# Performance work log

Measured on AMD Instinct MI355X. Metric: run time of the kernel, lower is better.

## Reference

```python
import jax, jax.numpy as jnp
import numpy as np

N_NODES = 50000
N_EDGES = 800000
IN_DIM, HID_DIM, N_CLASS = 128, 128, 2
DROPOUT_P = 0.5
NEG_SLOPE = 0.01  # F.leaky_relu default


def gcn_conv(x, src, dst, W, b, n_nodes):
    """PyG GCNConv: add self-loops, sym-normalize, aggregate, then bias."""
    loops = jnp.arange(n_nodes, dtype=src.dtype)
    s = jnp.concatenate([src, loops])
    d = jnp.concatenate([dst, loops])
    # degree on A + I (edge weights = 1), counted at destination
    deg = jax.ops.segment_sum(jnp.ones_like(d, dtype=x.dtype), d, num_segments=n_nodes)
    dis = jnp.where(deg > 0, jax.lax.rsqrt(deg), 0.0)  # deg^{-1/2}
    norm = dis[s] * dis[d]                               # [E+N]
    h = x @ W                                            # [N, out]
    msg = h[s] * norm[:, None]                           # gather + scale
    out = jax.ops.segment_sum(msg, d, num_segments=n_nodes)  # scatter-add
    return out + b


def dropout(x, p, key):
    keep = 1.0 - p
    mask = jax.random.bernoulli(key, keep, x.shape)
    return jnp.where(mask, x / keep, 0.0)


def setup_inputs() -> dict:
    key = jax.random.key(0)
    ks = jax.random.split(key, 8)
    x = jax.random.normal(ks[0], (N_NODES, IN_DIM), dtype=jnp.float32)
    edge_index = jax.random.randint(ks[1], (2, N_EDGES), 0, N_NODES, dtype=jnp.int64)
    def glorot(k, fin, fout):
        lim = np.sqrt(6.0 / (fin + fout)).astype(np.float32)
        return jax.random.uniform(k, (fin, fout), jnp.float32, -lim, lim)
    W1 = glorot(ks[2], IN_DIM, HID_DIM)
    W2 = glorot(ks[3], HID_DIM, HID_DIM)
    W3 = glorot(ks[4], HID_DIM, N_CLASS)
    b1 = jnp.zeros((HID_DIM,), jnp.float32)
    b2 = jnp.zeros((HID_DIM,), jnp.float32)
    b3 = jnp.zeros((N_CLASS,), jnp.float32)
    return {"x": x, "edge_index": edge_index, "W1": W1, "b1": b1,
            "W2": W2, "b2": b2, "W3": W3, "b3": b3}


def reference(x, edge_index, W1, b1, W2, b2, W3, b3):
    src, dst = edge_index[0], edge_index[1]
    n = x.shape[0]
    dkey = jax.random.key(42)
    k1, k2 = jax.random.split(dkey)
    h = gcn_conv(x, src, dst, W1, b1, n)
    h = jax.nn.leaky_relu(h, NEG_SLOPE)
    h = dropout(h, DROPOUT_P, k1)
    h = gcn_conv(h, src, dst, W2, b2, n)
    h = jax.nn.leaky_relu(h, NEG_SLOPE)
    h = dropout(h, DROPOUT_P, k2)
    h = gcn_conv(h, src, dst, W3, b3, n)
    return jax.nn.log_softmax(h, axis=1)
```

## Files before the change

kernel.cpp:

```cpp
#include <hip/hip_runtime.h>
#include <stdint.h>

#define N_NODES 50000
#define N_EDGES 800000
#define DIM     128
#define NB   196
#define CAP  8192
#define CHUNK 2048
#define NBLK 391
#define GNODES 16
#define GGRID 3125
#define GCAP2 2048
#define G3CAP 8192
#define ZBLK 98

typedef __attribute__((ext_vector_type(8))) unsigned short ushort8_t;
typedef __attribute__((ext_vector_type(8))) short bfrag;
typedef __attribute__((ext_vector_type(4))) float f32x4;

__host__ __device__ inline void threefry2x32(uint32_t k0, uint32_t k1,
                                             uint32_t x0, uint32_t x1,
                                             uint32_t& o0, uint32_t& o1) {
    uint32_t ks0 = k0, ks1 = k1, ks2 = k0 ^ k1 ^ 0x1BD11BDAu;
    uint32_t v0 = x0 + ks0, v1 = x1 + ks1;
#define TF_R(r) { v0 += v1; v1 = (v1 << (r)) | (v1 >> (32 - (r))); v1 ^= v0; }
    TF_R(13) TF_R(15) TF_R(26) TF_R(6)
    v0 += ks1; v1 += ks2 + 1u;
    TF_R(17) TF_R(29) TF_R(16) TF_R(24)
    v0 += ks2; v1 += ks0 + 2u;
    TF_R(13) TF_R(15) TF_R(26) TF_R(6)
    v0 += ks0; v1 += ks1 + 3u;
    TF_R(17) TF_R(29) TF_R(16) TF_R(24)
    v0 += ks1; v1 += ks2 + 4u;
    TF_R(13) TF_R(15) TF_R(26) TF_R(6)
    v0 += ks2; v1 += ks0 + 5u;
#undef TF_R
    o0 = v0; o1 = v1;
}

__device__ inline float drop_scale(uint32_t kk0, uint32_t kk1, uint32_t i) {
    uint32_t b0, b1;
    threefry2x32(kk0, kk1, 0u, i, b0, b1);
    uint32_t bits = b0 ^ b1;
    return (bits >> 31) ? 0.0f : 2.0f;
}

__device__ inline float bf2f(ushort u) {
    return __uint_as_float(((uint32_t)u) << 16);
}

__device__ inline ushort f2bf_rne(float f) {
    uint32_t bits = __float_as_uint(f);
    uint32_t lsb = (bits >> 16) & 1u;
    bits += 0x7fffu + lsb;
    return (ushort)(bits >> 16);
}

template<int F32A, int SCALE>
__device__ inline void gemm_body(const ushort* __restrict__ Xb,
                                 const float* __restrict__ Xf,
                                 const ushort* __restrict__ Wt,
                                 const float* __restrict__ dis,
                                 ushort* __restrict__ Hb, int gb, int tid) {
    int w = tid >> 6, lane = tid & 63;
    int m0 = gb * 128 + w * 32;
    int lrow = lane & 15, quad = lane >> 4;
    f32x4 acc[2][8] = {};
    for (int kt = 0; kt < DIM; kt += 32) {
        bfrag a[2], b[8];
        #pragma unroll
        for (int t = 0; t < 2; ++t) {
            int m = m0 + t * 16 + lrow;
            if (m >= N_NODES) m = 0;
            if (F32A) {
                const float* p = Xf + (size_t)m * DIM + kt + quad * 8;
                f32x4 v0 = *(const f32x4*)p;
                f32x4 v1 = *(const f32x4*)(p + 4);
                #pragma unroll
                for (int j = 0; j < 4; ++j) {
                    a[t][j]     = (short)f2bf_rne(v0[j]);
                    a[t][j + 4] = (short)f2bf_rne(v1[j]);
                }
            } else {
                a[t] = *(const bfrag*)(Xb + (size_t)m * DIM + kt + quad * 8);
            }
        }
        #pragma unroll
        for (int c = 0; c < 8; ++c) {
            int n = c * 16 + lrow;
            b[c] = *(const bfrag*)(Wt + (size_t)n * DIM + kt + quad * 8);
        }
        #pragma unroll
        for (int t = 0; t < 2; ++t)
            #pragma unroll
            for (int c = 0; c < 8; ++c)
                acc[t][c] = __builtin_amdgcn_mfma_f32_16x16x32_bf16(a[t], b[c], acc[t][c], 0, 0, 0);
    }
    #pragma unroll
    for (int t = 0; t < 2; ++t) {
        #pragma unroll
        for (int r = 0; r < 4; ++r) {
            int rowi = m0 + t * 16 + quad * 4 + r;
            if (rowi < N_NODES) {
                float dv = SCALE ? dis[rowi] : 1.0f;
                #pragma unroll
                for (int c = 0; c < 8; ++c) {
                    int feat = c * 16 + lrow;
                    float z = SCALE ? acc[t][c][r] * dv : acc[t][c][r];
                    Hb[(size_t)rowi * DIM + feat] = f2bf_rne(z);
                }
            }
        }
    }
}

__global__ __launch_bounds__(256) void k_prep(const float* __restrict__ W1,
                                              const float* __restrict__ W2,
                                              ushort* __restrict__ W1t,
                                              ushort* __restrict__ W2t,
                                              const int* __restrict__ src,
                                              const int* __restrict__ dst,
                                              uint32_t* __restrict__ gcur,
                                              uint32_t* __restrict__ packed,
                                              float* __restrict__ h3s) {
    __shared__ uint32_t h[NB];
    int b = blockIdx.x;
    int t = threadIdx.x;
    if (b < NBLK) {
        uint32_t dc[CHUNK / 256], sc[CHUNK / 256];
        if (t < NB) h[t] = 0u;
        __syncthreads();
        int base = b * CHUNK;
        #pragma unroll
        for (int i = 0; i < CHUNK / 256; ++i) {
            int e = base + i * 256 + t;
            if (e < N_EDGES) {
                dc[i] = (uint32_t)dst[e];
                sc[i] = (uint32_t)src[e];
                atomicAdd(&h[dc[i] >> 8], 1u);
            } else {
                dc[i] = 0xffffffffu;
            }
        }
        __syncthreads();
        if (t < NB) {
            uint32_t c = h[t];
            h[t] = c ? atomicAdd(&gcur[t], c) : 0u;
        }
        __syncthreads();
        #pragma unroll
        for (int i = 0; i < CHUNK / 256; ++i) {
            if (dc[i] != 0xffffffffu) {
                uint32_t d = dc[i];
                uint32_t s = sc[i];
                uint32_t bk = d >> 8;
                uint32_t pos = atomicAdd(&h[bk], 1u);
                if (pos < CAP)
                    packed[(size_t)bk * CAP + pos] = ((d & 255u) << 16) | s;
            }
        }
    } else if (b < NBLK + 128) {
        int j = (b - NBLK) * 256 + t;
        const float* W = (j < DIM * DIM) ? W1 : W2;
        ushort* Wt = (j < DIM * DIM) ? W1t : W2t;
        int i = j & (DIM * DIM - 1);
        int k = i >> 7, n = i & 127;
        Wt[n * DIM + k] = f2bf_rne(W[k * DIM + n]);
    } else {
        int idx = (b - NBLK - 128) * 256 + t;
        if (idx < (N_NODES * 2) / 4) {
            f32x4 z = {0.f, 0.f, 0.f, 0.f};
            ((f32x4*)h3s)[idx] = z;
        }
    }
}

__global__ __launch_bounds__(256) void k_fill(const uint32_t* __restrict__ gcur,
                                              const uint32_t* __restrict__ packed,
                                              uint32_t* __restrict__ row,
                                              float* __restrict__ dis,
                                              ushort* __restrict__ col16,
                                              const float* __restrict__ x,
                                              const ushort* __restrict__ W1t,
                                              ushort* __restrict__ Hb) {
    __shared__ uint32_t sdeg[256];
    __shared__ uint32_t scan[256];
    __shared__ uint32_t cur[256];
    int b = blockIdx.x;
    int t = threadIdx.x;
    if (b >= NB) {
        gemm_body<1, 0>(nullptr, x, W1t, nullptr, Hb, b - NB, t);
        return;
    }
    uint32_t n = gcur[b];
    scan[t] = (t < b) ? gcur[t] : 0u;
    __syncthreads();
    for (int off = 1; off < 256; off <<= 1) {
        uint32_t xx = (t >= off) ? scan[t - off] : 0u;
        __syncthreads();
        scan[t] += xx;
        __syncthreads();
    }
    uint32_t cbase = scan[255];
    __syncthreads();
    uint32_t pbase = (uint32_t)b * CAP;
    sdeg[t] = 0u;
    __syncthreads();
    for (uint32_t i = t; i < n; i += 256) {
        uint32_t u = packed[pbase + i];
        atomicAdd(&sdeg[u >> 16], 1u);
    }
    __syncthreads();
    uint32_t myd = sdeg[t];
    scan[t] = myd;
    __syncthreads();
    for (int off = 1; off < 256; off <<= 1) {
        uint32_t xx = (t >= off) ? scan[t - off] : 0u;
        __syncthreads();
        scan[t] += xx;
        __syncthreads();
    }
    uint32_t excl = scan[t] - myd;
    cur[t] = excl;
    int v = b * 256 + t;
    if (v <= N_NODES) row[v] = cbase + excl;
    if (v < N_NODES)  dis[v] = 1.0f / sqrtf((float)(myd + 1u));
    __syncthreads();
    for (uint32_t i = t; i < n; i += 256) {
        uint32_t u = packed[pbase + i];
        uint32_t pos = cbase + atomicAdd(&cur[u >> 16], 1u);
        col16[pos] = (ushort)(u & 0xffffu);
    }
}

template<int CLS, int SRCDIS>
__global__ __launch_bounds__(256) void k_gather_t(const uint32_t* __restrict__ row,
                                                  const ushort* __restrict__ col16,
                                                  const float* __restrict__ dis,
                                                  const ushort* __restrict__ Hb,
                                                  const float* __restrict__ bias,
                                                  ushort* __restrict__ OUTb,
                                                  const float* __restrict__ W3,
                                                  float* __restrict__ h3s,
                                                  uint32_t kk0, uint32_t kk1) {
    __shared__ ushort scol[GCAP2];
    __shared__ uint32_t srow[GNODES + 1];
    int tid = threadIdx.x;
    int nbase = blockIdx.x * GNODES;
    if (tid <= GNODES) srow[tid] = row[nbase + tid];
    __syncthreads();
    uint32_t eLo = srow[0];
    uint32_t count = srow[GNODES] - eLo;
    bool staged = count <= GCAP2;
    if (staged) {
        for (uint32_t i = tid; i < count; i += 256) scol[i] = col16[eLo + i];
    }
    __syncthreads();

    int nl = tid >> 4;
    int q  = tid & 15;
    int v = nbase + nl;
    float dv = dis[v];
    ushort8_t hv = *((const ushort8_t*)(Hb + (size_t)v * DIM + q * 8));
    float acc[8];
    #pragma unroll
    for (int j = 0; j < 8; ++j)
        acc[j] = SRCDIS ? dv * bf2f(hv[j]) : bf2f(hv[j]);

    uint32_t e0 = srow[nl] - eLo, e1 = srow[nl + 1] - eLo;
    uint32_t e = e0;
    if (staged) {
        for (; e + 4 <= e1; e += 4) {
            uint32_t s0 = scol[e], s1 = scol[e + 1], s2 = scol[e + 2], s3 = scol[e + 3];
            ushort8_t h0 = *((const ushort8_t*)(Hb + (size_t)s0 * DIM + q * 8));
            ushort8_t h1 = *((const ushort8_t*)(Hb + (size_t)s1 * DIM + q * 8));
            ushort8_t h2 = *((const ushort8_t*)(Hb + (size_t)s2 * DIM + q * 8));
            ushort8_t h3 = *((const ushort8_t*)(Hb + (size_t)s3 * DIM + q * 8));
            if (SRCDIS) {
                float d0 = dis[s0], d1 = dis[s1], d2 = dis[s2], d3 = dis[s3];
                #pragma unroll
                for (int j = 0; j < 8; ++j)
                    acc[j] += d0 * bf2f(h0[j]) + d1 * bf2f(h1[j])
                            + d2 * bf2f(h2[j]) + d3 * bf2f(h3[j]);
            } else {
                #pragma unroll
                for (int j = 0; j < 8; ++j)
                    acc[j] += (bf2f(h0[j]) + bf2f(h1[j])) + (bf2f(h2[j]) + bf2f(h3[j]));
            }
        }
        for (; e < e1; ++e) {
            uint32_t s0 = scol[e];
            ushort8_t h0 = *((const ushort8_t*)(Hb + (size_t)s0 * DIM + q * 8));
            float d0 = SRCDIS ? dis[s0] : 1.0f;
            #pragma unroll
            for (int j = 0; j < 8; ++j)
                acc[j] += SRCDIS ? d0 * bf2f(h0[j]) : bf2f(h0[j]);
        }
    } else {
        for (; e < e1; ++e) {
            uint32_t s0 = col16[eLo + e];
            ushort8_t h0 = *((const ushort8_t*)(Hb + (size_t)s0 * DIM + q * 8));
            float d0 = SRCDIS ? dis[s0] : 1.0f;
            #pragma unroll
            for (int j = 0; j < 8; ++j)
                acc[j] += SRCDIS ? d0 * bf2f(h0[j]) : bf2f(h0[j]);
        }
    }

    int cbase = q * 8;
    uint32_t ibase = (uint32_t)(v * DIM + cbase);
    if (CLS == 0) {
        ushort8_t o;
        #pragma unroll
        for (int j = 0; j < 8; ++j) {
            float z = acc[j] * dv + bias[cbase + j];
            z = (z >= 0.f) ? z : 0.01f * z;
            z *= drop_scale(kk0, kk1, ibase + j);
            o[j] = f2bf_rne(z);
        }
        *((ushort8_t*)(OUTb + (size_t)v * DIM + cbase)) = o;
    } else {
        float o0 = 0.f, o1 = 0.f;
        #pragma unroll
        for (int j = 0; j < 8; ++j) {
            float z = acc[j] * dv + bias[cbase + j];
            z = (z >= 0.f) ? z : 0.01f * z;
            z *= drop_scale(kk0, kk1, ibase + j);
            o0 += z * W3[(cbase + j) * 2 + 0];
            o1 += z * W3[(cbase + j) * 2 + 1];
        }
        o0 += __shfl_xor(o0, 1); o0 += __shfl_xor(o0, 2);
        o0 += __shfl_xor(o0, 4); o0 += __shfl_xor(o0, 8);
        o1 += __shfl_xor(o1, 1); o1 += __shfl_xor(o1, 2);
        o1 += __shfl_xor(o1, 4); o1 += __shfl_xor(o1, 8);
        if (q == 0) {
            atomicAdd(&h3s[v * 2 + 0], o0 * dv);
            atomicAdd(&h3s[v * 2 + 1], o1 * dv);
        }
    }
}

__global__ __launch_bounds__(256) void k_gemm_bf16(const ushort* __restrict__ Xb,
                                                   const ushort* __restrict__ Wt,
                                                   const float* __restrict__ dis,
                                                   ushort* __restrict__ Hb) {
    gemm_body<0, 1>(Xb, nullptr, Wt, dis, Hb, blockIdx.x, threadIdx.x);
}

__global__ __launch_bounds__(256) void k_gather3(const uint32_t* __restrict__ row,
                                                 const ushort* __restrict__ col16,
                                                 const float* __restrict__ dis,
                                                 const float* __restrict__ H3s,
                                                 const float* __restrict__ b3,
                                                 float* __restrict__ out) {
    __shared__ ushort scol[G3CAP];
    __shared__ uint32_t srow[257];
    int tid = threadIdx.x;
    int nbase = blockIdx.x * 256;
    int nend = nbase + 256; if (nend > N_NODES) nend = N_NODES;
    int nloc = nend - nbase;
    for (int i = tid; i <= nloc; i += 256) srow[i] = row[nbase + i];
    __syncthreads();
    uint32_t eLo = srow[0];
    uint32_t count = srow[nloc] - eLo;
    bool staged = count <= G3CAP;
    if (staged) {
        for (uint32_t i = tid; i < count; i += 256) scol[i] = col16[eLo + i];
    }
    __syncthreads();

    int v = nbase + tid;
    if (v >= N_NODES) return;
    const float2* H2 = (const float2*)H3s;
    float2 h = H2[v];
    float z0 = h.x, z1 = h.y;
    uint32_t e0 = srow[tid] - eLo, e1 = srow[tid + 1] - eLo;
    uint32_t e = e0;
    if (staged) {
        for (; e + 2 <= e1; e += 2) {
            float2 ha = H2[scol[e]];
            float2 hb = H2[scol[e + 1]];
            z0 += ha.x + hb.x; z1 += ha.y + hb.y;
        }
        if (e < e1) {
            float2 ha = H2[scol[e]];
            z0 += ha.x; z1 += ha.y;
        }
    } else {
        for (; e < e1; ++e) {
            float2 ha = H2[col16[eLo + e]];
            z0 += ha.x; z1 += ha.y;
        }
    }
    float dv = dis[v];
    z0 = z0 * dv + b3[0];
    z1 = z1 * dv + b3[1];
    float m = fmaxf(z0, z1);
    float lse = m + logf(expf(z0 - m) + expf(z1 - m));
    out[v * 2 + 0] = z0 - lse;
    out[v * 2 + 1] = z1 - lse;
}

extern "C" void kernel_launch(void* const* d_in, const int* in_sizes, int n_in,
                              void* d_out, int out_size, void* d_ws, size_t ws_size,
                              hipStream_t stream) {
    const float* x  = (const float*)d_in[0];
    const int*   ei = (const int*)d_in[1];
    const float* W1 = (const float*)d_in[2];
    const float* b1 = (const float*)d_in[3];
    const float* W2 = (const float*)d_in[4];
    const float* b2 = (const float*)d_in[5];
    const float* W3 = (const float*)d_in[6];
    const float* b3 = (const float*)d_in[7];
    float* out = (float*)d_out;

    const int* src = ei;
    const int* dst = ei + N_EDGES;

    uint32_t* wsu = (uint32_t*)d_ws;
    float*    wsf = (float*)d_ws;
    uint32_t* gcur   = wsu;
    uint32_t* row    = wsu + 256;
    float*    dis    = wsf + 50304;
    uint32_t* packed = wsu + 100352;
    ushort*   col16  = (ushort*)(wsu + 1705984);
    ushort*   Hb     = (ushort*)(wsu + 2106112);
    ushort*   Bb     = (ushort*)(wsu + 8506112);
    ushort*   W1t    = (ushort*)(wsu + 11706112);
    ushort*   W2t    = (ushort*)(wsu + 11714304);
    float*    h3s    = wsf + 11722496;

    uint32_t k1a, k1b, k2a, k2b;
    threefry2x32(0u, 42u, 0u, 0u, k1a, k1b);
    threefry2x32(0u, 42u, 0u, 1u, k2a, k2b);

    hipMemsetAsync(gcur, 0, 256 * sizeof(uint32_t), stream);

    k_prep<<<NBLK + 128 + ZBLK, 256, 0, stream>>>(W1, W2, W1t, W2t,
                                                  src, dst, gcur, packed, h3s);

    k_fill<<<NB + 391, 256, 0, stream>>>(gcur, packed, row, dis, col16,
                                         x, W1t, Hb);

    k_gather_t<0, 1><<<GGRID, 256, 0, stream>>>(row, col16, dis, Hb, b1, Bb,
                                                nullptr, nullptr, k1a, k1b);

    k_gemm_bf16<<<(N_NODES + 127) / 128, 256, 0, stream>>>(Bb, W2t, dis, Hb);
    k_gather_t<1, 0><<<GGRID, 256, 0, stream>>>(row, col16, dis, Hb, b2, nullptr,
                                                W3, h3s, k2a, k2b);

    k_gather3<<<(N_NODES + 255) / 256, 256, 0, stream>>>(row, col16, dis, h3s, b3, out);
}
```

Baseline: 215.3 us.

## Split hidden features into 32-wide panels and gather per panel for locality

The GEMM now writes the bf16 hidden matrix as four feature panels of 32 columns, each stored node-major. The gather kernel runs one block per panel for each group of 64 nodes, with 4 threads per node, so each pass only touches a 3.2MB slice of the table and should stay resident in cache. The final 2-class gather now uses two threads per node with a shuffle reduction. The cost is that edge indices are re-read once per panel and the layer-2 projection makes four atomic adds per node output instead of one.

```diff
diff --git a/kernel.cpp b/kernel.cpp
--- a/kernel.cpp
+++ b/kernel.cpp
@@ -8,10 +8,9 @@
 #define CAP  8192
 #define CHUNK 2048
 #define NBLK 391
-#define GNODES 16
-#define GGRID 3125
-#define GCAP2 2048
-#define G3CAP 8192
+#define GCAP 4096
+#define G3NODES 128
+#define G3CAP 4096
 #define ZBLK 98
 
 typedef __attribute__((ext_vector_type(8))) unsigned short ushort8_t;
@@ -106,8 +105,9 @@
                 #pragma unroll
                 for (int c = 0; c < 8; ++c) {
                     int feat = c * 16 + lrow;
+                    int fp = feat >> 5, off = feat & 31;
                     float z = SCALE ? acc[t][c][r] * dv : acc[t][c][r];
-                    Hb[(size_t)rowi * DIM + feat] = f2bf_rne(z);
+                    Hb[((size_t)fp * N_NODES + rowi) * 32 + off] = f2bf_rne(z);
                 }
             }
         }
@@ -243,25 +243,31 @@
                                                   const float* __restrict__ W3,
                                                   float* __restrict__ h3s,
                                                   uint32_t kk0, uint32_t kk1) {
-    __shared__ ushort scol[GCAP2];
-    __shared__ uint32_t srow[GNODES + 1];
+    __shared__ ushort scol[GCAP];
+    __shared__ uint32_t srow[65];
+    int fp = blockIdx.x & 3;
+    int c = blockIdx.x >> 2;
     int tid = threadIdx.x;
-    int nbase = blockIdx.x * GNODES;
-    if (tid <= GNODES) srow[tid] = row[nbase + tid];
+    int nbase = c * 64;
+    int nend = nbase + 64; if (nend > N_NODES) nend = N_NODES;
+    int nloc = nend - nbase;
+    for (int i = tid; i <= nloc; i += 256) srow[i] = row[nbase + i];
     __syncthreads();
     uint32_t eLo = srow[0];
-    uint32_t count = srow[GNODES] - eLo;
-    bool staged = count <= GCAP2;
+    uint32_t count = srow[nloc] - eLo;
+    bool staged = count <= GCAP;
     if (staged) {
         for (uint32_t i = tid; i < count; i += 256) scol[i] = col16[eLo + i];
     }
     __syncthreads();
 
-    int nl = tid >> 4;
-    int q  = tid & 15;
+    int nl = tid >> 2;
+    int q  = tid & 3;
     int v = nbase + nl;
+    if (v >= N_NODES) return;
     float dv = dis[v];
-    ushort8_t hv = *((const ushort8_t*)(Hb + (size_t)v * DIM + q * 8));
+    const ushort* Hf = Hb + (size_t)fp * N_NODES * 32;
+    ushort8_t hv = *((const ushort8_t*)(Hf + (size_t)v * 32 + q * 8));
     float acc[8];
     #pragma unroll
     for (int j = 0; j < 8; ++j)
@@ -272,10 +278,10 @@
     if (staged) {
         for (; e + 4 <= e1; e += 4) {
             uint32_t s0 = scol[e], s1 = scol[e + 1], s2 = scol[e + 2], s3 = scol[e + 3];
-            ushort8_t h0 = *((const ushort8_t*)(Hb + (size_t)s0 * DIM + q * 8));
-            ushort8_t h1 = *((const ushort8_t*)(Hb + (size_t)s1 * DIM + q * 8));
-            ushort8_t h2 = *((const ushort8_t*)(Hb + (size_t)s2 * DIM + q * 8));
-            ushort8_t h3 = *((const ushort8_t*)(Hb + (size_t)s3 * DIM + q * 8));
+            ushort8_t h0 = *((const ushort8_t*)(Hf + (size_t)s0 * 32 + q * 8));
+            ushort8_t h1 = *((const ushort8_t*)(Hf + (size_t)s1 * 32 + q * 8));
+            ushort8_t h2 = *((const ushort8_t*)(Hf + (size_t)s2 * 32 + q * 8));
+            ushort8_t h3 = *((const ushort8_t*)(Hf + (size_t)s3 * 32 + q * 8));
             if (SRCDIS) {
                 float d0 = dis[s0], d1 = dis[s1], d2 = dis[s2], d3 = dis[s3];
                 #pragma unroll
@@ -290,7 +296,7 @@
         }
         for (; e < e1; ++e) {
             uint32_t s0 = scol[e];
-            ushort8_t h0 = *((const ushort8_t*)(Hb + (size_t)s0 * DIM + q * 8));
+            ushort8_t h0 = *((const ushort8_t*)(Hf + (size_t)s0 * 32 + q * 8));
             float d0 = SRCDIS ? dis[s0] : 1.0f;
             #pragma unroll
             for (int j = 0; j < 8; ++j)
@@ -299,7 +305,7 @@
     } else {
         for (; e < e1; ++e) {
             uint32_t s0 = col16[eLo + e];
-            ushort8_t h0 = *((const ushort8_t*)(Hb + (size_t)s0 * DIM + q * 8));
+            ushort8_t h0 = *((const ushort8_t*)(Hf + (size_t)s0 * 32 + q * 8));
             float d0 = SRCDIS ? dis[s0] : 1.0f;
             #pragma unroll
             for (int j = 0; j < 8; ++j)
@@ -307,7 +313,7 @@
         }
     }
 
-    int cbase = q * 8;
+    int cbase = fp * 32 + q * 8;
     uint32_t ibase = (uint32_t)(v * DIM + cbase);
     if (CLS == 0) {
         ushort8_t o;
@@ -330,9 +336,7 @@
             o1 += z * W3[(cbase + j) * 2 + 1];
         }
         o0 += __shfl_xor(o0, 1); o0 += __shfl_xor(o0, 2);
-        o0 += __shfl_xor(o0, 4); o0 += __shfl_xor(o0, 8);
         o1 += __shfl_xor(o1, 1); o1 += __shfl_xor(o1, 2);
-        o1 += __shfl_xor(o1, 4); o1 += __shfl_xor(o1, 8);
         if (q == 0) {
             atomicAdd(&h3s[v * 2 + 0], o0 * dv);
             atomicAdd(&h3s[v * 2 + 1], o1 * dv);
@@ -354,10 +358,10 @@
                                                  const float* __restrict__ b3,
                                                  float* __restrict__ out) {
     __shared__ ushort scol[G3CAP];
-    __shared__ uint32_t srow[257];
+    __shared__ uint32_t srow[G3NODES + 1];
     int tid = threadIdx.x;
-    int nbase = blockIdx.x * 256;
-    int nend = nbase + 256; if (nend > N_NODES) nend = N_NODES;
+    int nbase = blockIdx.x * G3NODES;
+    int nend = nbase + G3NODES; if (nend > N_NODES) nend = N_NODES;
     int nloc = nend - nbase;
     for (int i = tid; i <= nloc; i += 256) srow[i] = row[nbase + i];
     __syncthreads();
@@ -369,29 +373,31 @@
     }
     __syncthreads();
 
-    int v = nbase + tid;
+    int nl = tid >> 1;
+    int par = tid & 1;
+    int v = nbase + nl;
     if (v >= N_NODES) return;
     const float2* H2 = (const float2*)H3s;
-    float2 h = H2[v];
-    float z0 = h.x, z1 = h.y;
-    uint32_t e0 = srow[tid] - eLo, e1 = srow[tid + 1] - eLo;
-    uint32_t e = e0;
+    float z0 = 0.f, z1 = 0.f;
+    if (par == 0) {
+        float2 h = H2[v];
+        z0 = h.x; z1 = h.y;
+    }
+    uint32_t e0 = srow[nl] - eLo, e1 = srow[nl + 1] - eLo;
     if (staged) {
-        for (; e + 2 <= e1; e += 2) {
-            float2 ha = H2[scol[e]];
-            float2 hb = H2[scol[e + 1]];
-            z0 += ha.x + hb.x; z1 += ha.y + hb.y;
-        }
-        if (e < e1) {
+        for (uint32_t e = e0 + par; e < e1; e += 2) {
             float2 ha = H2[scol[e]];
             z0 += ha.x; z1 += ha.y;
         }
     } else {
-        for (; e < e1; ++e) {
+        for (uint32_t e = e0 + par; e < e1; e += 2) {
             float2 ha = H2[col16[eLo + e]];
             z0 += ha.x; z1 += ha.y;
         }
     }
+    z0 += __shfl_xor(z0, 1);
+    z1 += __shfl_xor(z1, 1);
+    if (par) return;
     float dv = dis[v];
     z0 = z0 * dv + b3[0];
     z1 = z1 * dv + b3[1];
@@ -442,12 +448,15 @@
     k_fill<<<NB + 391, 256, 0, stream>>>(gcur, packed, row, dis, col16,
                                          x, W1t, Hb);
 
-    k_gather_t<0, 1><<<GGRID, 256, 0, stream>>>(row, col16, dis, Hb, b1, Bb,
+    int ggrid = ((N_NODES + 63) / 64) * 4;
+
+    k_gather_t<0, 1><<<ggrid, 256, 0, stream>>>(row, col16, dis, Hb, b1, Bb,
                                                 nullptr, nullptr, k1a, k1b);
 
     k_gemm_bf16<<<(N_NODES + 127) / 128, 256, 0, stream>>>(Bb, W2t, dis, Hb);
-    k_gather_t<1, 0><<<GGRID, 256, 0, stream>>>(row, col16, dis, Hb, b2, nullptr,
+    k_gather_t<1, 0><<<ggrid, 256, 0, stream>>>(row, col16, dis, Hb, b2, nullptr,
                                                 W3, h3s, k2a, k2b);
 
-    k_gather3<<<(N_NODES + 255) / 256, 256, 0, stream>>>(row, col16, dis, h3s, b3, out);
-}
+    k_gather3<<<(N_NODES + G3NODES - 1) / G3NODES, 256, 0, stream>>>(row, col16, dis,
+                                                                     h3s, b3, out);
+}
```

After: 219.9 us. 2.2% more time.
